# Kernel tuning notes

Measured on AMD Instinct MI355X. Metric: run time of the kernel, lower is better.

## Reference

```python
import jax, jax.numpy as jnp
import numpy as np
import math

NUM_HEADS = 4

def _mha(x, in_w, in_b, out_w, out_b, key_mask):
    # x: [V, S, B, E] (seq-first per-frame role tokens), key_mask: [V, S] True=valid role
    V, S, B, E = x.shape
    hd = E // NUM_HEADS
    qkv = jnp.einsum('vsbe,fe->vsbf', x, in_w) + in_b  # torch Linear: x @ W.T
    q, k, v = jnp.split(qkv, 3, axis=-1)
    q = q.reshape(V, S, B, NUM_HEADS, hd) * (1.0 / math.sqrt(hd))
    k = k.reshape(V, S, B, NUM_HEADS, hd)
    v = v.reshape(V, S, B, NUM_HEADS, hd)
    scores = jnp.einsum('vsbhd,vtbhd->vbhst', q, k)
    scores = jnp.where(key_mask[:, None, None, None, :], scores, -jnp.inf)
    w = jax.nn.softmax(scores, axis=-1)
    o = jnp.einsum('vbhst,vtbhd->vsbhd', w, v).reshape(V, S, B, E)
    return jnp.einsum('vsbe,fe->vsbf', o, out_w) + out_b

def setup_inputs() -> dict:
    B, D, V, R, H, MR, G, L = 16, 2048, 504, 190, 32, 6, 2000, 3
    rng = np.random.default_rng(0)
    verb_roles = np.full((V, MR), -1, dtype=np.int32)  # ragged frames, -1 padded (pad_v_r)
    for vi in range(V):
        n = int(rng.integers(1, MR + 1))
        verb_roles[vi, :n] = rng.choice(R, size=n, replace=False)
    group_len = rng.integers(G // 4, G + 1, size=R).astype(np.int32)  # |r_n[r]| per role
    key = jax.random.key(0)
    ks = jax.random.split(key, 6)
    f = jnp.float32
    return dict(
        rep=jax.random.normal(ks[0], (B, D), f),
        W_v=jax.random.normal(ks[1], (D, V), f) / math.sqrt(D),
        b_v=jnp.zeros((V,), f),
        W_r=jax.random.normal(ks[2], (D, R * H), f) / math.sqrt(D),
        b_r=jnp.zeros((R * H,), f),
        attn_in_w=jax.random.normal(ks[3], (L, 3 * H, H), f) / math.sqrt(H),
        attn_in_b=jnp.zeros((L, 3 * H), f),
        attn_out_w=jax.random.normal(ks[4], (L, H, H), f) / math.sqrt(H),
        attn_out_b=jnp.zeros((L, H), f),
        W_n=jax.random.normal(ks[5], (R, H, G), f) / math.sqrt(H),
        b_n=jnp.zeros((R, G), f),
        verb_roles=jnp.asarray(verb_roles),
        group_len=jnp.asarray(group_len),
    )

def reference(rep, W_v, b_v, W_r, b_r, attn_in_w, attn_in_b, attn_out_w, attn_out_b,
              W_n, b_n, verb_roles, group_len):
    B = rep.shape[0]
    V, MR = verb_roles.shape
    R, H, G = W_n.shape
    v_potential = rep @ W_v + b_v                     # [B, V]  linear_v
    node = (rep @ W_r + b_r).reshape(B, R, H)         # [B, R, H]  linear_r
    pos_mask = verb_roles >= 0                        # [V, MR] valid-role mask
    ridx = jnp.maximum(verb_roles, 0)                 # safe gather index
    # gather per-frame role reps: [V, MR, B, H] (seq-first like torch MHA)
    x = jnp.transpose(node[:, ridx, :], (1, 2, 0, 3))
    for l in range(attn_in_w.shape[0]):               # 3 self-attention layers
        x = _mha(x, attn_in_w[l], attn_in_b[l], attn_out_w[l], attn_out_b[l], pos_mask)
    # per-role grouped noun logits (linear_n[r]), ragged groups masked to -inf
    logits = jnp.einsum('vsbh,vshg->vsbg', x, W_n[ridx]) + b_n[ridx][:, :, None, :]  # [V,MR,B,G]
    gmask = jnp.arange(G)[None, None, :] < group_len[ridx][:, :, None]               # [V,MR,G]
    ml = jnp.where(gmask[:, :, None, :], logits, -jnp.inf)
    mmax = jnp.max(ml, axis=-1)                       # [V,MR,B] per-role max (log_sum_exp's max)
    maxi = jnp.argmax(ml, axis=-1)                    # local noun index within group
    lse = mmax + jnp.log(jnp.sum(jnp.exp(ml - mmax[..., None]), axis=-1))
    pm = pos_mask[:, :, None]                         # F.pad(..., value=0) on padded roles
    lse = jnp.where(pm, lse, 0.0)
    mmax = jnp.where(pm, mmax, 0.0)
    maxi = jnp.where(pm, maxi, 0)
    vrn_marginal = jnp.transpose(lse, (2, 0, 1))      # [B, V, MR]
    vr_max = jnp.transpose(mmax, (2, 0, 1))
    vr_maxi = jnp.transpose(maxi, (2, 0, 1))
    v_marginal = vrn_marginal.sum(-1) + v_potential   # [B, V]
    m = jnp.max(v_marginal, axis=1)
    norm = m + jnp.log(jnp.sum(jnp.exp(v_marginal - m[:, None]), axis=1))  # [B]
    v_max = vr_max.sum(-1) + v_potential              # max_max prediction scores
    return (v_potential, norm, v_max, vrn_marginal, vr_max, vr_maxi)
```

## Files before the change

### kernel.cpp

```cpp
#include <hip/hip_runtime.h>
#include <math.h>

constexpr int kB = 16;
constexpr int kD = 2048;
constexpr int kV = 504;
constexpr int kR = 190;
constexpr int kH = 32;
constexpr int kMR = 6;
constexpr int kG = 2000;
constexpr int kL = 3;
constexpr int kNH = 4;
constexpr int kHD = 8;
constexpr int kC1 = kV + kR * kH;
constexpr int kNDS = 8;
constexpr int kDCH = kD / kNDS;

constexpr int kQS = 100;

constexpr int kMAXP = 64;
constexpr int kGCH = 500;
constexpr int kGC = 4;

constexpr size_t WS_NODE = 0;
constexpr size_t WS_X    = WS_NODE + (size_t)kB*kR*kH;
constexpr size_t WS_REST = WS_X + (size_t)kV*kMR*kB*kH;
constexpr size_t WS_PART = WS_REST;
constexpr size_t WS_PM   = WS_REST;
constexpr size_t WS_PS   = WS_PM + (size_t)kV*kMR*kB*kGC;
constexpr size_t WS_PI   = WS_PS + (size_t)kV*kMR*kB*kGC;
constexpr size_t WS_CNT  = WS_PI + (size_t)kV*kMR*kB*kGC;
constexpr size_t WS_PAIR = WS_CNT + kR;

constexpr size_t O_VPOT = 0;
constexpr size_t O_NORM = O_VPOT + (size_t)kB*kV;
constexpr size_t O_VMAX = O_NORM + kB;
constexpr size_t O_VRN  = O_VMAX + (size_t)kB*kV;
constexpr size_t O_VRM  = O_VRN + (size_t)kB*kV*kMR;
constexpr size_t O_VRI  = O_VRM + (size_t)kB*kV*kMR;

__device__ inline float dot4(float4 a, float4 w, float acc) {
  return fmaf(a.x, w.x, fmaf(a.y, w.y, fmaf(a.z, w.z, fmaf(a.w, w.w, acc))));
}

__global__ __launch_bounds__(256) void k1a(const float* __restrict__ rep,
                                           const float* __restrict__ Wv,
                                           const float* __restrict__ Wr,
                                           float* __restrict__ part) {
  __shared__ float rl[kB][kDCH];
  const int tid = threadIdx.x;
  const int col = blockIdx.x * 256 + tid;
  const int d0 = blockIdx.y * kDCH;
  for (int i = tid; i < kB * kDCH; i += 256) {
    int b = i >> 8, dd = i & (kDCH - 1);
    rl[b][dd] = rep[b * kD + d0 + dd];
  }
  __syncthreads();
  if (col >= kC1) return;
  const float* Wp;
  int stride;
  if (col < kV) { Wp = Wv + (size_t)d0 * kV + col; stride = kV; }
  else          { Wp = Wr + (size_t)d0 * (kR*kH) + (col - kV); stride = kR*kH; }
  float acc[kB];
#pragma unroll
  for (int b = 0; b < kB; b++) acc[b] = 0.f;
  for (int dd = 0; dd < kDCH; dd++) {
    float w = Wp[(size_t)dd * stride];
#pragma unroll
    for (int b = 0; b < kB; b++) acc[b] += rl[b][dd] * w;
  }
  float* p = part + (size_t)(blockIdx.y * kB) * kC1 + col;
#pragma unroll
  for (int b = 0; b < kB; b++) p[(size_t)b * kC1] = acc[b];
}

__global__ __launch_bounds__(256) void k1b(const float* __restrict__ part,
                                           const float* __restrict__ bv,
                                           const float* __restrict__ br,
                                           float* __restrict__ out,
                                           float* __restrict__ node) {
  int idx = blockIdx.x * 256 + threadIdx.x;
  if (idx >= kB * kC1) return;
  int b = idx / kC1, col = idx % kC1;
  float s = 0.f;
#pragma unroll
  for (int ds = 0; ds < kNDS; ds++) s += part[(size_t)(ds * kB + b) * kC1 + col];
  if (col < kV) out[O_VPOT + (size_t)b * kV + col] = s + bv[col];
  else          node[(size_t)b * (kR*kH) + (col - kV)] = s + br[col - kV];
}

__global__ __launch_bounds__(256) void k0(const int* __restrict__ verb_roles,
                                          int* __restrict__ cnt,
                                          int* __restrict__ pairs) {
  const int tid = threadIdx.x;
  for (int i = tid; i < kR; i += 256) cnt[i] = 0;
  __syncthreads();
  for (int i = tid; i < kV * kMR; i += 256) {
    int r = verb_roles[i];
    if (r >= 0) {
      int pos = atomicAdd(&cnt[r], 1);
      if (pos < kMAXP) pairs[r * kMAXP + pos] = i;
    }
  }
}

__global__ __launch_bounds__(384) void k2(const float* __restrict__ node,
                                          const int* __restrict__ verb_roles,
                                          const float* __restrict__ in_w,
                                          const float* __restrict__ in_b,
                                          const float* __restrict__ out_w,
                                          const float* __restrict__ out_b,
                                          float* __restrict__ xout) {
  __shared__ float wi[96 * 44];
  __shared__ float wo[32 * 44];
  __shared__ float bi[96];
  __shared__ float bo[32];
  __shared__ float qkv[96 * kQS];
  __shared__ int roles[kMR];
  const int v = blockIdx.x;
  const int tid = threadIdx.x;
  if (tid < kMR) roles[tid] = verb_roles[v * kMR + tid];
  __syncthreads();
  const int rp = tid >> 3, oct = tid & 7;
  const int row0 = 2 * rp, row1 = row0 + 1;
  const int s0 = row0 >> 4, b0 = row0 & 15;
  const int s1 = row1 >> 4, b1 = row1 & 15;
  float4 xr[2][8];
  {
    int r0 = roles[s0] < 0 ? 0 : roles[s0];
    int r1 = roles[s1] < 0 ? 0 : roles[s1];
    const float4* xp0 = (const float4*)(node + (size_t)b0 * (kR*kH) + r0 * kH);
    const float4* xp1 = (const float4*)(node + (size_t)b1 * (kR*kH) + r1 * kH);
#pragma unroll
    for (int j = 0; j < 8; j++) { xr[0][j] = xp0[j]; xr[1][j] = xp1[j]; }
  }
  for (int l = 0; l < kL; l++) {
    for (int i = tid; i < 96 * 32; i += 384) wi[(i >> 5) * 44 + (i & 31)] = in_w[(size_t)l*96*32 + i];
    for (int i = tid; i < 32 * 32; i += 384) wo[(i >> 5) * 44 + (i & 31)] = out_w[(size_t)l*32*32 + i];
    if (tid < 96) bi[tid] = in_b[l*96 + tid];
    else if (tid < 128) bo[tid - 96] = out_b[l*32 + (tid - 96)];
    __syncthreads();
#pragma unroll
    for (int fi = 0; fi < 12; fi++) {
      const int f = oct + 8 * fi;
      const float4* wr = (const float4*)&wi[f * 44];
      float a0 = 0.f, a1 = 0.f, a2 = 0.f, a3 = 0.f;
      float c0 = 0.f, c1 = 0.f, c2 = 0.f, c3 = 0.f;
#pragma unroll
      for (int j = 0; j < 8; j += 4) {
        float4 w0 = wr[j], w1 = wr[j+1], w2 = wr[j+2], w3 = wr[j+3];
        a0 = dot4(xr[0][j],   w0, a0);  c0 = dot4(xr[1][j],   w0, c0);
        a1 = dot4(xr[0][j+1], w1, a1);  c1 = dot4(xr[1][j+1], w1, c1);
        a2 = dot4(xr[0][j+2], w2, a2);  c2 = dot4(xr[1][j+2], w2, c2);
        a3 = dot4(xr[0][j+3], w3, a3);  c3 = dot4(xr[1][j+3], w3, c3);
      }
      const float bf = bi[f];
      qkv[row0 * kQS + f] = ((a0 + a1) + (a2 + a3)) + bf;
      qkv[row1 * kQS + f] = ((c0 + c1) + (c2 + c3)) + bf;
    }
    __syncthreads();
    {
      const int us = tid >> 6, uh = (tid >> 4) & 3, ub = tid & 15;
      const int base = (us * 16 + ub) * kQS + uh * 8;
      float q[8];
#pragma unroll
      for (int d = 0; d < 8; d++) q[d] = qkv[base + d] * 0.35355339059327373f;
      float sc[kMR];
      float mx = -INFINITY;
#pragma unroll
      for (int t = 0; t < kMR; t++) {
        const int kb = (t * 16 + ub) * kQS + 32 + uh * 8;
        float a = 0.f;
#pragma unroll
        for (int d = 0; d < 8; d++) a = fmaf(q[d], qkv[kb + d], a);
        sc[t] = a;
        if (roles[t] >= 0 && a > mx) mx = a;
      }
      float sum = 0.f;
#pragma unroll
      for (int t = 0; t < kMR; t++) {
        float e = (roles[t] >= 0) ? __expf(sc[t] - mx) : 0.f;
        sc[t] = e; sum += e;
      }
      const float inv = 1.f / sum;
      float o[8];
#pragma unroll
      for (int d = 0; d < 8; d++) o[d] = 0.f;
#pragma unroll
      for (int t = 0; t < kMR; t++) {
        const float w = sc[t] * inv;
        const int vb = (t * 16 + ub) * kQS + 64 + uh * 8;
#pragma unroll
        for (int d = 0; d < 8; d++) o[d] = fmaf(w, qkv[vb + d], o[d]);
      }
#pragma unroll
      for (int d = 0; d < 8; d++) qkv[base + d] = o[d];
    }
    __syncthreads();
    {
      const float4* o0 = (const float4*)&qkv[row0 * kQS];
      const float4* o1 = (const float4*)&qkv[row1 * kQS];
#pragma unroll
      for (int j = 0; j < 8; j++) { xr[0][j] = o0[j]; xr[1][j] = o1[j]; }
    }
    float acc0[4], acc1[4];
#pragma unroll
    for (int ci = 0; ci < 4; ci++) {
      const int c2 = oct + 8 * ci;
      const float4* wr = (const float4*)&wo[c2 * 44];
      float a0 = 0.f, a1 = 0.f, a2 = 0.f, a3 = 0.f;
      float d0 = 0.f, d1 = 0.f, d2 = 0.f, d3 = 0.f;
#pragma unroll
      for (int j = 0; j < 8; j += 4) {
        float4 w0 = wr[j], w1 = wr[j+1], w2 = wr[j+2], w3 = wr[j+3];
        a0 = dot4(xr[0][j],   w0, a0);  d0 = dot4(xr[1][j],   w0, d0);
        a1 = dot4(xr[0][j+1], w1, a1);  d1 = dot4(xr[1][j+1], w1, d1);
        a2 = dot4(xr[0][j+2], w2, a2);  d2 = dot4(xr[1][j+2], w2, d2);
        a3 = dot4(xr[0][j+3], w3, a3);  d3 = dot4(xr[1][j+3], w3, d3);
      }
      const float bc = bo[c2];
      acc0[ci] = ((a0 + a1) + (a2 + a3)) + bc;
      acc1[ci] = ((d0 + d1) + (d2 + d3)) + bc;
    }
#pragma unroll
    for (int ci = 0; ci < 4; ci++) {
      qkv[row0 * kQS + 32 + oct + 8 * ci] = acc0[ci];
      qkv[row1 * kQS + 32 + oct + 8 * ci] = acc1[ci];
    }
    __syncthreads();
    if (l < kL - 1) {
      const float4* n0 = (const float4*)&qkv[row0 * kQS + 32];
      const float4* n1 = (const float4*)&qkv[row1 * kQS + 32];
#pragma unroll
      for (int j = 0; j < 8; j++) { xr[0][j] = n0[j]; xr[1][j] = n1[j]; }
      __syncthreads();
    }
  }
  for (int i = tid; i < 96 * 32; i += 384) {
    const int row = i >> 5, h = i & 31;
    xout[(size_t)v * (96 * 32) + i] = qkv[row * kQS + 32 + h];
  }
}

__global__ __launch_bounds__(256) void k3a(const float* __restrict__ xw,
                                           const int* __restrict__ cnt,
                                           const int* __restrict__ pairs,
                                           const int* __restrict__ group_len,
                                           const float* __restrict__ Wn,
                                           const float* __restrict__ bn,
                                           float* __restrict__ PM,
                                           float* __restrict__ PS,
                                           float* __restrict__ PI) {
  __shared__ float Wl[kGCH * 36];
  __shared__ float Bl[kGCH];
  __shared__ float mbM[4][8][kB], mbS[4][8][kB], mbI[4][8][kB];
  const int r = blockIdx.x, gc = blockIdx.y;
  const int glen = group_len[r];
  const int g0 = gc * kGCH;
  if (g0 >= glen) return;
  int c = cnt[r]; if (c > kMAXP) c = kMAXP;
  if (c == 0) return;
  const int gn = (kGCH < glen - g0) ? kGCH : (glen - g0);
  const int tid = threadIdx.x;
  const float* W = Wn + (size_t)r * kH * kG + g0;
  const float* bias = bn + (size_t)r * kG + g0;
  for (int g = tid; g < gn; g += 256) {
#pragma unroll
    for (int h = 0; h < kH; h++) Wl[g * 36 + h] = W[(size_t)h * kG + g];
    Bl[g] = bias[g];
  }
  __syncthreads();
  const int wave = tid >> 6, lane = tid & 63;
  const int b = lane & 15, slot = lane >> 4;
  int gw0 = wave * 125, gw1 = gw0 + 125;
  gw0 = (gw0 < gn) ? gw0 : gn;
  gw1 = (gw1 < gn) ? gw1 : gn;
  const int nq = (c + 7) >> 3;
  for (int q = 0; q < nq; q++) {
    const int p0 = 8 * q + 2 * slot, p1 = p0 + 1;
    const bool v0 = p0 < c, v1 = p1 < c;
    const int pr0 = pairs[r * kMAXP + (v0 ? p0 : 0)];
    const int pr1 = pairs[r * kMAXP + (v1 ? p1 : 0)];
    float4 x0[8], x1[8];
    {
      const float4* xp0 = (const float4*)(xw + ((size_t)pr0 * kB + b) * kH);
      const float4* xp1 = (const float4*)(xw + ((size_t)pr1 * kB + b) * kH);
#pragma unroll
      for (int j = 0; j < 8; j++) { x0[j] = xp0[j]; x1[j] = xp1[j]; }
    }
    float m0 = -INFINITY, s0 = 0.f, m1 = -INFINITY, s1 = 0.f;
    int i0 = 0, i1 = 0;
#pragma unroll 2
    for (int g = gw0; g < gw1; g++) {
      const float4* wr = (const float4*)&Wl[g * 36];
      const float bg = Bl[g];
      float a0 = 0.f, a1 = 0.f, a2 = 0.f, a3 = 0.f;
      float c0 = 0.f, c1 = 0.f, c2 = 0.f, c3 = 0.f;
#pragma unroll
      for (int j = 0; j < 8; j += 4) {
        float4 w0 = wr[j], w1 = wr[j+1], w2 = wr[j+2], w3 = wr[j+3];
        a0 = dot4(x0[j],   w0, a0);  c0 = dot4(x1[j],   w0, c0);
        a1 = dot4(x0[j+1], w1, a1);  c1 = dot4(x1[j+1], w1, c1);
        a2 = dot4(x0[j+2], w2, a2);  c2 = dot4(x1[j+2], w2, c2);
        a3 = dot4(x0[j+3], w3, a3);  c3 = dot4(x1[j+3], w3, c3);
      }
      const float acc0 = ((a0 + a1) + (a2 + a3)) + bg;
      const float acc1 = ((c0 + c1) + (c2 + c3)) + bg;
      {
        float d = acc0 - m0; bool gt = d > 0.f;
        float e = __expf(gt ? -d : d);
        s0 = gt ? fmaf(s0, e, 1.f) : s0 + e;
        i0 = gt ? g0 + g : i0;  m0 = gt ? acc0 : m0;
      }
      {
        float d = acc1 - m1; bool gt = d > 0.f;
        float e = __expf(gt ? -d : d);
        s1 = gt ? fmaf(s1, e, 1.f) : s1 + e;
        i1 = gt ? g0 + g : i1;  m1 = gt ? acc1 : m1;
      }
    }
    mbM[wave][2*slot][b]   = v0 ? m0 : -INFINITY;
    mbS[wave][2*slot][b]   = s0;
    mbI[wave][2*slot][b]   = (float)i0;
    mbM[wave][2*slot+1][b] = v1 ? m1 : -INFINITY;
    mbS[wave][2*slot+1][b] = s1;
    mbI[wave][2*slot+1][b] = (float)i1;
    __syncthreads();
    if (tid < 128) {
      const int pl = tid >> 4, bb = tid & 15;
      const int pg = 8 * q + pl;
      if (pg < c) {
        float M = -INFINITY, S = 0.f; int I = 0;
#pragma unroll
        for (int w = 0; w < 4; w++) {
          float om = mbM[w][pl][bb];
          float os = mbS[w][pl][bb];
          int oi = (int)mbI[w][pl][bb];
          if (om != -INFINITY) {
            if (M == -INFINITY)      { M = om; S = os; I = oi; }
            else if (om > M)         { S = S * __expf(M - om) + os; M = om; I = oi; }
            else if (om < M)         { S = S + os * __expf(om - M); }
            else                     { S += os; I = (oi < I) ? oi : I; }
          }
        }
        const int pr2 = pairs[r * kMAXP + pg];
        size_t o = ((size_t)pr2 * kB + bb) * kGC + gc;
        PM[o] = M; PS[o] = S; PI[o] = (float)I;
      }
    }
    __syncthreads();
  }
}

__device__ inline void lse_merge(float& m, float& s, int& i, float om, float os, int oi) {
  if (om == -INFINITY) return;
  if (m == -INFINITY) { m = om; s = os; i = oi; return; }
  if (om > m)       { s = s * __expf(m - om) + os; m = om; i = oi; }
  else if (om < m)  { s = s + os * __expf(om - m); }
  else              { s += os; i = (oi < i) ? oi : i; }
}

__global__ __launch_bounds__(256) void k3b(const int* __restrict__ verb_roles,
                                           const int* __restrict__ group_len,
                                           const float* __restrict__ PM,
                                           const float* __restrict__ PS,
                                           const float* __restrict__ PI,
                                           float* __restrict__ out) {
  const int idx = blockIdx.x * 256 + threadIdx.x;
  if (idx >= kV * kMR * kB) return;
  const int pr = idx >> 4;
  const int b = idx & 15;
  const int v = pr / kMR, s = pr % kMR;
  const size_t o = ((size_t)b * kV + v) * kMR + s;
  const int r = verb_roles[pr];
  if (r < 0) {
    out[O_VRN + o] = 0.f; out[O_VRM + o] = 0.f; out[O_VRI + o] = 0.f;
    return;
  }
  const int glen = group_len[r];
  const int ngc = (glen + kGCH - 1) / kGCH;
  float M = -INFINITY, S = 0.f; int I = 0;
  for (int gc = 0; gc < ngc; gc++) {
    size_t po = ((size_t)pr * kB + b) * kGC + gc;
    lse_merge(M, S, I, PM[po], PS[po], (int)PI[po]);
  }
  out[O_VRN + o] = M + logf(S);
  out[O_VRM + o] = M;
  out[O_VRI + o] = (float)I;
}

__global__ __launch_bounds__(256) void k4(float* __restrict__ out) {
  const int b = blockIdx.x;
  const int tid = threadIdx.x;
  float M = -INFINITY, S = 0.f;
  for (int v = tid; v < kV; v += 256) {
    float sm = 0.f, sx = 0.f;
#pragma unroll
    for (int s = 0; s < kMR; s++) {
      size_t o = ((size_t)b * kV + v) * kMR + s;
      sm += out[O_VRN + o];
      sx += out[O_VRM + o];
    }
    float vp = out[O_VPOT + (size_t)b * kV + v];
    float vm = sm + vp;
    out[O_VMAX + (size_t)b * kV + v] = sx + vp;
    float nm = fmaxf(M, vm);
    S = S * __expf(M - nm) + __expf(vm - nm);
    M = nm;
  }
#pragma unroll
  for (int off = 1; off < 64; off <<= 1) {
    float om = __shfl_xor(M, off);
    float os = __shfl_xor(S, off);
    if (om != -INFINITY) {
      if (M == -INFINITY) { M = om; S = os; }
      else if (om > M) { S = S * __expf(M - om) + os; M = om; }
      else { S += os * __expf(om - M); }
    }
  }
  __shared__ float rm2[4], rs2[4];
  const int wave = tid >> 6, lane = tid & 63;
  if (lane == 0) { rm2[wave] = M; rs2[wave] = S; }
  __syncthreads();
  if (tid == 0) {
    float Mm = rm2[0], Ss = rs2[0];
    for (int w = 1; w < 4; w++) {
      float om = rm2[w], os = rs2[w];
      if (om > Mm) { Ss = Ss * __expf(Mm - om) + os; Mm = om; }
      else { Ss += os * __expf(om - Mm); }
    }
    out[O_NORM + b] = Mm + logf(Ss);
  }
}

extern "C" void kernel_launch(void* const* d_in, const int* in_sizes, int n_in,
                              void* d_out, int out_size, void* d_ws, size_t ws_size,
                              hipStream_t stream) {
  const float* rep = (const float*)d_in[0];
  const float* Wv  = (const float*)d_in[1];
  const float* bv  = (const float*)d_in[2];
  const float* Wr  = (const float*)d_in[3];
  const float* br  = (const float*)d_in[4];
  const float* aiw = (const float*)d_in[5];
  const float* aib = (const float*)d_in[6];
  const float* aow = (const float*)d_in[7];
  const float* aob = (const float*)d_in[8];
  const float* Wn  = (const float*)d_in[9];
  const float* bnn = (const float*)d_in[10];
  const int* vrl   = (const int*)d_in[11];
  const int* gl    = (const int*)d_in[12];
  float* out = (float*)d_out;
  float* ws  = (float*)d_ws;
  int* icnt  = (int*)(ws + WS_CNT);
  int* ipair = (int*)(ws + WS_PAIR);

  k1a<<<dim3((kC1 + 255) / 256, kNDS), 256, 0, stream>>>(rep, Wv, Wr, ws + WS_PART);
  k1b<<<(kB * kC1 + 255) / 256, 256, 0, stream>>>(ws + WS_PART, bv, br, out, ws + WS_NODE);
  k0<<<1, 256, 0, stream>>>(vrl, icnt, ipair);
  k2<<<kV, 384, 0, stream>>>(ws + WS_NODE, vrl, aiw, aib, aow, aob, ws + WS_X);
  k3a<<<dim3(kR, kGC), 256, 0, stream>>>(ws + WS_X, icnt, ipair, gl, Wn, bnn,
                                         ws + WS_PM, ws + WS_PS, ws + WS_PI);
  k3b<<<(kV * kMR * kB + 255) / 256, 256, 0, stream>>>(vrl, gl, ws + WS_PM, ws + WS_PS,
                                                       ws + WS_PI, out);
  k4<<<kB, 256, 0, stream>>>(out);
}
```

Baseline: 227.6 us.

## Register-block four role pairs per thread in noun scoring kernel, retune group chunking

The noun-logit kernel now has each thread handle four (verb,role) pairs instead of two. Each weight row it loads from shared memory is reused across four dot products, which cuts LDS traffic per FMA and halves the number of pair-batch iterations. The group dimension is also split into five chunks of 448 instead of four of 500, and a two-blocks-per-CU launch bound is requested. In exchange, register pressure rises from holding four x vectors (128 floats), which may cause spills under the occupancy hint.

```diff
diff --git a/kernel.cpp b/kernel.cpp
--- a/kernel.cpp
+++ b/kernel.cpp
@@ -18,8 +18,8 @@
 constexpr int kQS = 100;
 
 constexpr int kMAXP = 64;
-constexpr int kGCH = 500;
-constexpr int kGC = 4;
+constexpr int kGCH = 448;
+constexpr int kGC = 5;
 
 constexpr size_t WS_NODE = 0;
 constexpr size_t WS_X    = WS_NODE + (size_t)kB*kR*kH;
@@ -241,18 +241,18 @@
   }
 }
 
-__global__ __launch_bounds__(256) void k3a(const float* __restrict__ xw,
-                                           const int* __restrict__ cnt,
-                                           const int* __restrict__ pairs,
-                                           const int* __restrict__ group_len,
-                                           const float* __restrict__ Wn,
-                                           const float* __restrict__ bn,
-                                           float* __restrict__ PM,
-                                           float* __restrict__ PS,
-                                           float* __restrict__ PI) {
+__global__ __launch_bounds__(256, 2) void k3a(const float* __restrict__ xw,
+                                              const int* __restrict__ cnt,
+                                              const int* __restrict__ pairs,
+                                              const int* __restrict__ group_len,
+                                              const float* __restrict__ Wn,
+                                              const float* __restrict__ bn,
+                                              float* __restrict__ PM,
+                                              float* __restrict__ PS,
+                                              float* __restrict__ PI) {
   __shared__ float Wl[kGCH * 36];
   __shared__ float Bl[kGCH];
-  __shared__ float mbM[4][8][kB], mbS[4][8][kB], mbI[4][8][kB];
+  __shared__ float mbM[4][16][kB], mbS[4][16][kB], mbI[4][16][kB];
   const int r = blockIdx.x, gc = blockIdx.y;
   const int glen = group_len[r];
   const int g0 = gc * kGCH;
@@ -271,63 +271,61 @@
   __syncthreads();
   const int wave = tid >> 6, lane = tid & 63;
   const int b = lane & 15, slot = lane >> 4;
-  int gw0 = wave * 125, gw1 = gw0 + 125;
+  int gw0 = wave * 112, gw1 = gw0 + 112;
   gw0 = (gw0 < gn) ? gw0 : gn;
   gw1 = (gw1 < gn) ? gw1 : gn;
-  const int nq = (c + 7) >> 3;
+  const int nq = (c + 15) >> 4;
   for (int q = 0; q < nq; q++) {
-    const int p0 = 8 * q + 2 * slot, p1 = p0 + 1;
-    const bool v0 = p0 < c, v1 = p1 < c;
-    const int pr0 = pairs[r * kMAXP + (v0 ? p0 : 0)];
-    const int pr1 = pairs[r * kMAXP + (v1 ? p1 : 0)];
-    float4 x0[8], x1[8];
+    const int pbase = 16 * q + 4 * slot;
+    bool valid[4];
+    float4 x[4][8];
+#pragma unroll
+    for (int k = 0; k < 4; k++) {
+      const int p = pbase + k;
+      valid[k] = p < c;
+      const int pr = pairs[r * kMAXP + (valid[k] ? p : 0)];
+      const float4* xp = (const float4*)(xw + ((size_t)pr * kB + b) * kH);
+#pragma unroll
+      for (int j = 0; j < 8; j++) x[k][j] = xp[j];
+    }
+    float m[4], s[4]; int ix[4];
+#pragma unroll
+    for (int k = 0; k < 4; k++) { m[k] = -INFINITY; s[k] = 0.f; ix[k] = 0; }
+    for (int g = gw0; g < gw1; g++) {
+      float4 w[8];
+      const float4* wr = (const float4*)&Wl[g * 36];
+#pragma unroll
+      for (int j = 0; j < 8; j++) w[j] = wr[j];
+      const float bg = Bl[g];
+#pragma unroll
+      for (int k = 0; k < 4; k++) {
+        float a0 = 0.f, a1 = 0.f, a2 = 0.f, a3 = 0.f;
+#pragma unroll
+        for (int j = 0; j < 8; j += 4) {
+          a0 = dot4(x[k][j],   w[j],   a0);
+          a1 = dot4(x[k][j+1], w[j+1], a1);
+          a2 = dot4(x[k][j+2], w[j+2], a2);
+          a3 = dot4(x[k][j+3], w[j+3], a3);
+        }
+        const float acc = ((a0 + a1) + (a2 + a3)) + bg;
+        const float d = acc - m[k];
+        const bool gt = d > 0.f;
+        const float e = __expf(gt ? -d : d);
+        s[k] = gt ? fmaf(s[k], e, 1.f) : s[k] + e;
+        ix[k] = gt ? g0 + g : ix[k];
+        m[k] = gt ? acc : m[k];
+      }
+    }
+#pragma unroll
+    for (int k = 0; k < 4; k++) {
+      mbM[wave][4*slot + k][b] = valid[k] ? m[k] : -INFINITY;
+      mbS[wave][4*slot + k][b] = s[k];
+      mbI[wave][4*slot + k][b] = (float)ix[k];
+    }
+    __syncthreads();
     {
-      const float4* xp0 = (const float4*)(xw + ((size_t)pr0 * kB + b) * kH);
-      const float4* xp1 = (const float4*)(xw + ((size_t)pr1 * kB + b) * kH);
-#pragma unroll
-      for (int j = 0; j < 8; j++) { x0[j] = xp0[j]; x1[j] = xp1[j]; }
-    }
-    float m0 = -INFINITY, s0 = 0.f, m1 = -INFINITY, s1 = 0.f;
-    int i0 = 0, i1 = 0;
-#pragma unroll 2
-    for (int g = gw0; g < gw1; g++) {
-      const float4* wr = (const float4*)&Wl[g * 36];
-      const float bg = Bl[g];
-      float a0 = 0.f, a1 = 0.f, a2 = 0.f, a3 = 0.f;
-      float c0 = 0.f, c1 = 0.f, c2 = 0.f, c3 = 0.f;
-#pragma unroll
-      for (int j = 0; j < 8; j += 4) {
-        float4 w0 = wr[j], w1 = wr[j+1], w2 = wr[j+2], w3 = wr[j+3];
-        a0 = dot4(x0[j],   w0, a0);  c0 = dot4(x1[j],   w0, c0);
-        a1 = dot4(x0[j+1], w1, a1);  c1 = dot4(x1[j+1], w1, c1);
-        a2 = dot4(x0[j+2], w2, a2);  c2 = dot4(x1[j+2], w2, c2);
-        a3 = dot4(x0[j+3], w3, a3);  c3 = dot4(x1[j+3], w3, c3);
-      }
-      const float acc0 = ((a0 + a1) + (a2 + a3)) + bg;
-      const float acc1 = ((c0 + c1) + (c2 + c3)) + bg;
-      {
-        float d = acc0 - m0; bool gt = d > 0.f;
-        float e = __expf(gt ? -d : d);
-        s0 = gt ? fmaf(s0, e, 1.f) : s0 + e;
-        i0 = gt ? g0 + g : i0;  m0 = gt ? acc0 : m0;
-      }
-      {
-        float d = acc1 - m1; bool gt = d > 0.f;
-        float e = __expf(gt ? -d : d);
-        s1 = gt ? fmaf(s1, e, 1.f) : s1 + e;
-        i1 = gt ? g0 + g : i1;  m1 = gt ? acc1 : m1;
-      }
-    }
-    mbM[wave][2*slot][b]   = v0 ? m0 : -INFINITY;
-    mbS[wave][2*slot][b]   = s0;
-    mbI[wave][2*slot][b]   = (float)i0;
-    mbM[wave][2*slot+1][b] = v1 ? m1 : -INFINITY;
-    mbS[wave][2*slot+1][b] = s1;
-    mbI[wave][2*slot+1][b] = (float)i1;
-    __syncthreads();
-    if (tid < 128) {
       const int pl = tid >> 4, bb = tid & 15;
-      const int pg = 8 * q + pl;
+      const int pg = 16 * q + pl;
       if (pg < c) {
         float M = -INFINITY, S = 0.f; int I = 0;
 #pragma unroll
```

After: 240.1 us. 1.06x slower.

## Stream W_n tiles through small LDS sub-chunks to raise k3a occupancy

Applied to the files above, without the earlier changes.

The noun-logit kernel k3a stops staging its whole 500-column W_n chunk in shared memory. It now uses 400-column chunks spread over 5 grid slices and reloads 100-column sub-tiles inside the pair loop, which cuts LDS use from about 72KB to about 16KB per block. Launch bounds request 4 blocks per CU. The trade-off is that W_n sub-tiles are re-read from global/L2 once per group of 8 pairs (nq times) rather than once per block, and two extra barriers are added per sub-tile. Row loads are now coalesced along g rather than strided across h.

```diff
diff --git a/kernel.cpp b/kernel.cpp
--- a/kernel.cpp
+++ b/kernel.cpp
@@ -18,8 +18,9 @@
 constexpr int kQS = 100;
 
 constexpr int kMAXP = 64;
-constexpr int kGCH = 500;
-constexpr int kGC = 4;
+constexpr int kGCH = 400;
+constexpr int kGC = 5;
+constexpr int kSUB = 100;
 
 constexpr size_t WS_NODE = 0;
 constexpr size_t WS_X    = WS_NODE + (size_t)kB*kR*kH;
@@ -241,17 +242,17 @@
   }
 }
 
-__global__ __launch_bounds__(256) void k3a(const float* __restrict__ xw,
-                                           const int* __restrict__ cnt,
-                                           const int* __restrict__ pairs,
-                                           const int* __restrict__ group_len,
-                                           const float* __restrict__ Wn,
-                                           const float* __restrict__ bn,
-                                           float* __restrict__ PM,
-                                           float* __restrict__ PS,
-                                           float* __restrict__ PI) {
-  __shared__ float Wl[kGCH * 36];
-  __shared__ float Bl[kGCH];
+__global__ __launch_bounds__(256, 4) void k3a(const float* __restrict__ xw,
+                                              const int* __restrict__ cnt,
+                                              const int* __restrict__ pairs,
+                                              const int* __restrict__ group_len,
+                                              const float* __restrict__ Wn,
+                                              const float* __restrict__ bn,
+                                              float* __restrict__ PM,
+                                              float* __restrict__ PS,
+                                              float* __restrict__ PI) {
+  __shared__ float Wl[kSUB * 36];
+  __shared__ float Bl[kSUB];
   __shared__ float mbM[4][8][kB], mbS[4][8][kB], mbI[4][8][kB];
   const int r = blockIdx.x, gc = blockIdx.y;
   const int glen = group_len[r];
@@ -261,19 +262,10 @@
   if (c == 0) return;
   const int gn = (kGCH < glen - g0) ? kGCH : (glen - g0);
   const int tid = threadIdx.x;
+  const int wave = tid >> 6, lane = tid & 63;
+  const int b = lane & 15, slot = lane >> 4;
   const float* W = Wn + (size_t)r * kH * kG + g0;
   const float* bias = bn + (size_t)r * kG + g0;
-  for (int g = tid; g < gn; g += 256) {
-#pragma unroll
-    for (int h = 0; h < kH; h++) Wl[g * 36 + h] = W[(size_t)h * kG + g];
-    Bl[g] = bias[g];
-  }
-  __syncthreads();
-  const int wave = tid >> 6, lane = tid & 63;
-  const int b = lane & 15, slot = lane >> 4;
-  int gw0 = wave * 125, gw1 = gw0 + 125;
-  gw0 = (gw0 < gn) ? gw0 : gn;
-  gw1 = (gw1 < gn) ? gw1 : gn;
   const int nq = (c + 7) >> 3;
   for (int q = 0; q < nq; q++) {
     const int p0 = 8 * q + 2 * slot, p1 = p0 + 1;
@@ -289,33 +281,53 @@
     }
     float m0 = -INFINITY, s0 = 0.f, m1 = -INFINITY, s1 = 0.f;
     int i0 = 0, i1 = 0;
-#pragma unroll 2
-    for (int g = gw0; g < gw1; g++) {
-      const float4* wr = (const float4*)&Wl[g * 36];
-      const float bg = Bl[g];
-      float a0 = 0.f, a1 = 0.f, a2 = 0.f, a3 = 0.f;
-      float c0 = 0.f, c1 = 0.f, c2 = 0.f, c3 = 0.f;
-#pragma unroll
-      for (int j = 0; j < 8; j += 4) {
-        float4 w0 = wr[j], w1 = wr[j+1], w2 = wr[j+2], w3 = wr[j+3];
-        a0 = dot4(x0[j],   w0, a0);  c0 = dot4(x1[j],   w0, c0);
-        a1 = dot4(x0[j+1], w1, a1);  c1 = dot4(x1[j+1], w1, c1);
-        a2 = dot4(x0[j+2], w2, a2);  c2 = dot4(x1[j+2], w2, c2);
-        a3 = dot4(x0[j+3], w3, a3);  c3 = dot4(x1[j+3], w3, c3);
-      }
-      const float acc0 = ((a0 + a1) + (a2 + a3)) + bg;
-      const float acc1 = ((c0 + c1) + (c2 + c3)) + bg;
-      {
-        float d = acc0 - m0; bool gt = d > 0.f;
-        float e = __expf(gt ? -d : d);
-        s0 = gt ? fmaf(s0, e, 1.f) : s0 + e;
-        i0 = gt ? g0 + g : i0;  m0 = gt ? acc0 : m0;
-      }
-      {
-        float d = acc1 - m1; bool gt = d > 0.f;
-        float e = __expf(gt ? -d : d);
-        s1 = gt ? fmaf(s1, e, 1.f) : s1 + e;
-        i1 = gt ? g0 + g : i1;  m1 = gt ? acc1 : m1;
+#pragma unroll
+    for (int sub = 0; sub < kGCH / kSUB; sub++) {
+      const int sb = sub * kSUB;
+      __syncthreads();
+      for (int i = tid; i < kSUB * 33; i += 256) {
+        if (i < kSUB * 32) {
+          const int h = i / kSUB;
+          const int g = i - h * kSUB;
+          Wl[g * 36 + h] = W[(size_t)h * kG + sb + g];
+        } else {
+          const int g = i - kSUB * 32;
+          Bl[g] = bias[sb + g];
+        }
+      }
+      __syncthreads();
+      int gwa = wave * (kSUB / 4), gwb = gwa + (kSUB / 4);
+      const int sn = (sb < gn) ? ((gn - sb < kSUB) ? gn - sb : kSUB) : 0;
+      gwa = (gwa < sn) ? gwa : sn;
+      gwb = (gwb < sn) ? gwb : sn;
+      for (int g = gwa; g < gwb; g++) {
+        const float4* wr = (const float4*)&Wl[g * 36];
+        const float bg = Bl[g];
+        const int gabs = g0 + sb + g;
+        float a0 = 0.f, a1 = 0.f, a2 = 0.f, a3 = 0.f;
+        float c0 = 0.f, c1 = 0.f, c2 = 0.f, c3 = 0.f;
+#pragma unroll
+        for (int j = 0; j < 8; j += 4) {
+          float4 w0 = wr[j], w1 = wr[j+1], w2 = wr[j+2], w3 = wr[j+3];
+          a0 = dot4(x0[j],   w0, a0);  c0 = dot4(x1[j],   w0, c0);
+          a1 = dot4(x0[j+1], w1, a1);  c1 = dot4(x1[j+1], w1, c1);
+          a2 = dot4(x0[j+2], w2, a2);  c2 = dot4(x1[j+2], w2, c2);
+          a3 = dot4(x0[j+3], w3, a3);  c3 = dot4(x1[j+3], w3, c3);
+        }
+        const float acc0 = ((a0 + a1) + (a2 + a3)) + bg;
+        const float acc1 = ((c0 + c1) + (c2 + c3)) + bg;
+        {
+          float d = acc0 - m0; bool gt = d > 0.f;
+          float e = __expf(gt ? -d : d);
+          s0 = gt ? fmaf(s0, e, 1.f) : s0 + e;
+          i0 = gt ? gabs : i0;  m0 = gt ? acc0 : m0;
+        }
+        {
+          float d = acc1 - m1; bool gt = d > 0.f;
+          float e = __expf(gt ? -d : d);
+          s1 = gt ? fmaf(s1, e, 1.f) : s1 + e;
+          i1 = gt ? gabs : i1;  m1 = gt ? acc1 : m1;
+        }
       }
     }
     mbM[wave][2*slot][b]   = v0 ? m0 : -INFINITY;
```

Measured after the change: 307.8 us. +35.2%, slower.

## Split k3a pair quads across grid z and batch online-softmax over 8 logits

Applied to the files above, without the earlier changes.

Adds a third grid dimension so two blocks per (role, group-chunk) process alternating pair quads, increasing block-level parallelism. The inner noun loop now computes 8 logits, takes a local max/argmax and sum of exps, then merges into the running state, shortening the serial dependency chain of the online log-sum-exp. Costs: each block reloads the same weight chunk into shared memory (duplicate global traffic), and the merge uses extra exps.

```diff
diff --git a/kernel.cpp b/kernel.cpp
--- a/kernel.cpp
+++ b/kernel.cpp
@@ -253,12 +253,14 @@
   __shared__ float Wl[kGCH * 36];
   __shared__ float Bl[kGCH];
   __shared__ float mbM[4][8][kB], mbS[4][8][kB], mbI[4][8][kB];
-  const int r = blockIdx.x, gc = blockIdx.y;
+  const int r = blockIdx.x, gc = blockIdx.y, z = blockIdx.z;
   const int glen = group_len[r];
   const int g0 = gc * kGCH;
   if (g0 >= glen) return;
   int c = cnt[r]; if (c > kMAXP) c = kMAXP;
   if (c == 0) return;
+  const int nq = (c + 7) >> 3;
+  if (z >= nq) return;
   const int gn = (kGCH < glen - g0) ? kGCH : (glen - g0);
   const int tid = threadIdx.x;
   const float* W = Wn + (size_t)r * kH * kG + g0;
@@ -274,8 +276,7 @@
   int gw0 = wave * 125, gw1 = gw0 + 125;
   gw0 = (gw0 < gn) ? gw0 : gn;
   gw1 = (gw1 < gn) ? gw1 : gn;
-  const int nq = (c + 7) >> 3;
-  for (int q = 0; q < nq; q++) {
+  for (int q = z; q < nq; q += 2) {
     const int p0 = 8 * q + 2 * slot, p1 = p0 + 1;
     const bool v0 = p0 < c, v1 = p1 < c;
     const int pr0 = pairs[r * kMAXP + (v0 ? p0 : 0)];
@@ -289,34 +290,48 @@
     }
     float m0 = -INFINITY, s0 = 0.f, m1 = -INFINITY, s1 = 0.f;
     int i0 = 0, i1 = 0;
-#pragma unroll 2
-    for (int g = gw0; g < gw1; g++) {
-      const float4* wr = (const float4*)&Wl[g * 36];
-      const float bg = Bl[g];
-      float a0 = 0.f, a1 = 0.f, a2 = 0.f, a3 = 0.f;
-      float c0 = 0.f, c1 = 0.f, c2 = 0.f, c3 = 0.f;
-#pragma unroll
-      for (int j = 0; j < 8; j += 4) {
-        float4 w0 = wr[j], w1 = wr[j+1], w2 = wr[j+2], w3 = wr[j+3];
-        a0 = dot4(x0[j],   w0, a0);  c0 = dot4(x1[j],   w0, c0);
-        a1 = dot4(x0[j+1], w1, a1);  c1 = dot4(x1[j+1], w1, c1);
-        a2 = dot4(x0[j+2], w2, a2);  c2 = dot4(x1[j+2], w2, c2);
-        a3 = dot4(x0[j+3], w3, a3);  c3 = dot4(x1[j+3], w3, c3);
-      }
-      const float acc0 = ((a0 + a1) + (a2 + a3)) + bg;
-      const float acc1 = ((c0 + c1) + (c2 + c3)) + bg;
-      {
-        float d = acc0 - m0; bool gt = d > 0.f;
-        float e = __expf(gt ? -d : d);
-        s0 = gt ? fmaf(s0, e, 1.f) : s0 + e;
-        i0 = gt ? g0 + g : i0;  m0 = gt ? acc0 : m0;
-      }
-      {
-        float d = acc1 - m1; bool gt = d > 0.f;
-        float e = __expf(gt ? -d : d);
-        s1 = gt ? fmaf(s1, e, 1.f) : s1 + e;
-        i1 = gt ? g0 + g : i1;  m1 = gt ? acc1 : m1;
-      }
+    for (int gg = gw0; gg < gw1; gg += 8) {
+      float l0[8], l1[8];
+#pragma unroll
+      for (int j = 0; j < 8; j++) {
+        const int g = gg + j;
+        const bool in = g < gw1;
+        const float4* wr = (const float4*)&Wl[(in ? g : gw0) * 36];
+        const float bg = Bl[in ? g : gw0];
+        float a0 = 0.f, a1 = 0.f, a2 = 0.f, a3 = 0.f;
+        float c0 = 0.f, c1 = 0.f, c2 = 0.f, c3 = 0.f;
+#pragma unroll
+        for (int jj = 0; jj < 8; jj += 4) {
+          float4 w0 = wr[jj], w1 = wr[jj+1], w2 = wr[jj+2], w3 = wr[jj+3];
+          a0 = dot4(x0[jj],   w0, a0);  c0 = dot4(x1[jj],   w0, c0);
+          a1 = dot4(x0[jj+1], w1, a1);  c1 = dot4(x1[jj+1], w1, c1);
+          a2 = dot4(x0[jj+2], w2, a2);  c2 = dot4(x1[jj+2], w2, c2);
+          a3 = dot4(x0[jj+3], w3, a3);  c3 = dot4(x1[jj+3], w3, c3);
+        }
+        l0[j] = in ? (((a0 + a1) + (a2 + a3)) + bg) : -INFINITY;
+        l1[j] = in ? (((c0 + c1) + (c2 + c3)) + bg) : -INFINITY;
+      }
+      float gm0 = l0[0], gm1 = l1[0];
+      int gi0 = 0, gi1 = 0;
+#pragma unroll
+      for (int j = 1; j < 8; j++) {
+        bool t0 = l0[j] > gm0; gm0 = t0 ? l0[j] : gm0; gi0 = t0 ? j : gi0;
+        bool t1 = l1[j] > gm1; gm1 = t1 ? l1[j] : gm1; gi1 = t1 ? j : gi1;
+      }
+      float e00 = __expf(l0[0]-gm0), e01 = __expf(l0[1]-gm0),
+            e02 = __expf(l0[2]-gm0), e03 = __expf(l0[3]-gm0),
+            e04 = __expf(l0[4]-gm0), e05 = __expf(l0[5]-gm0),
+            e06 = __expf(l0[6]-gm0), e07 = __expf(l0[7]-gm0);
+      float e10 = __expf(l1[0]-gm1), e11 = __expf(l1[1]-gm1),
+            e12 = __expf(l1[2]-gm1), e13 = __expf(l1[3]-gm1),
+            e14 = __expf(l1[4]-gm1), e15 = __expf(l1[5]-gm1),
+            e16 = __expf(l1[6]-gm1), e17 = __expf(l1[7]-gm1);
+      float t0 = ((e00+e01)+(e02+e03)) + ((e04+e05)+(e06+e07));
+      float t1 = ((e10+e11)+(e12+e13)) + ((e14+e15)+(e16+e17));
+      if (gm0 > m0) { s0 = fmaf(s0, __expf(m0 - gm0), t0); m0 = gm0; i0 = g0 + gg + gi0; }
+      else          { s0 = fmaf(t0, __expf(gm0 - m0), s0); }
+      if (gm1 > m1) { s1 = fmaf(s1, __expf(m1 - gm1), t1); m1 = gm1; i1 = g0 + gg + gi1; }
+      else          { s1 = fmaf(t1, __expf(gm1 - m1), s1); }
     }
     mbM[wave][2*slot][b]   = v0 ? m0 : -INFINITY;
     mbS[wave][2*slot][b]   = s0;
@@ -457,8 +472,8 @@
   k1b<<<(kB * kC1 + 255) / 256, 256, 0, stream>>>(ws + WS_PART, bv, br, out, ws + WS_NODE);
   k0<<<1, 256, 0, stream>>>(vrl, icnt, ipair);
   k2<<<kV, 384, 0, stream>>>(ws + WS_NODE, vrl, aiw, aib, aow, aob, ws + WS_X);
-  k3a<<<dim3(kR, kGC), 256, 0, stream>>>(ws + WS_X, icnt, ipair, gl, Wn, bnn,
-                                         ws + WS_PM, ws + WS_PS, ws + WS_PI);
+  k3a<<<dim3(kR, kGC, 2), 256, 0, stream>>>(ws + WS_X, icnt, ipair, gl, Wn, bnn,
+                                            ws + WS_PM, ws + WS_PS, ws + WS_PI);
   k3b<<<(kV * kMR * kB + 255) / 256, 256, 0, stream>>>(vrl, gl, ws + WS_PM, ws + WS_PS,
                                                        ws + WS_PI, out);
   k4<<<kB, 256, 0, stream>>>(out);
```

New measurement: 318.0 us. 1.4x slower.
